# Kernel tuning notes

Measured on AMD Instinct MI355X. Metric: run time of the kernel, lower is better.

## Reference

```python
import jax, jax.numpy as jnp
import numpy as np

N = 50000    # nodes
R = 3        # relations
E = 600000   # edges per relation
IN, HID, OUT = 128, 64, 64


def setup_inputs() -> dict:
    key = jax.random.key(0)
    k = jax.random.split(key, 5)
    x = jax.random.normal(k[0], (N, IN), dtype=jnp.float32)
    src = jax.random.randint(k[1], (R, E), 0, N, dtype=jnp.int32)
    dst = jax.random.randint(k[2], (R, E), 0, N, dtype=jnp.int32)
    # glorot-ish init like dgl.nn.GraphConv weight; bias init zeros
    W1 = jax.random.normal(k[3], (R, IN, HID), dtype=jnp.float32) * (IN ** -0.5)
    b1 = jnp.zeros((R, HID), dtype=jnp.float32)
    W2 = jax.random.normal(k[4], (R, HID, OUT), dtype=jnp.float32) * (HID ** -0.5)
    b2 = jnp.zeros((R, OUT), dtype=jnp.float32)
    return {"x": x, "W1": W1, "b1": b1, "W2": W2, "b2": b2, "src": src, "dst": dst}


def _graph_conv(x, src, dst, W, b):
    """dgl.nn.GraphConv with norm='both', single relation.
    x: [N, Fin]; src/dst: [E] int; W: [Fin, Fout]; b: [Fout].
    """
    n = x.shape[0]
    ones = jnp.ones(src.shape[0], dtype=x.dtype)
    out_deg = jax.ops.segment_sum(ones, src, num_segments=n)
    h = x * (jnp.maximum(out_deg, 1.0) ** -0.5)[:, None]   # src-side norm
    if W.shape[0] > W.shape[1]:
        # mult W first, then aggregate (fewer flops per edge)
        h = h @ W
        agg = jax.ops.segment_sum(h[src], dst, num_segments=n)  # [N, Fout]
    else:
        agg = jax.ops.segment_sum(h[src], dst, num_segments=n) @ W
    in_deg = jax.ops.segment_sum(ones, dst, num_segments=n)
    return agg * (jnp.maximum(in_deg, 1.0) ** -0.5)[:, None] + b


def _hetero_conv(x, src, dst, W, b):
    # HeteroGraphConv(aggregate='sum'): run each relation's GraphConv, sum results.
    per_rel = jax.vmap(_graph_conv, in_axes=(None, 0, 0, 0, 0))(x, src, dst, W, b)
    return per_rel.sum(axis=0)  # [N, Fout]


def reference(x, W1, b1, W2, b2, src, dst):
    h = jax.nn.relu(_hetero_conv(x, src, dst, W1, b1))
    return _hetero_conv(h, src, dst, W2, b2)
```

## Files before the change

kernel.cpp:

```cpp
#include <hip/hip_runtime.h>

#define NODES 50000
#define RELS  3
#define NEDGE 600000
#define FIN   128
#define FHID  64
#define FOUT  64
#define SEGS  (RELS * NODES)

#define HC     96
#define HCHUNK (NEDGE / HC)
#define HBYTES NODES
#define HWORDS (HBYTES / 4)

#define BS     250
#define NBUK   200
#define NBUKT  (RELS * NBUK)
#define CAPLOG 12
#define CAP    (1 << CAPLOG)
#define BCH    192
#define BCHUNK (NEDGE / BCH)

typedef _Float16 half8 __attribute__((ext_vector_type(8)));
typedef float   floatx4 __attribute__((ext_vector_type(4)));

__global__ __launch_bounds__(1024) void hist_kernel(const int* __restrict__ src,
                                                    unsigned int* __restrict__ slab32,
                                                    int* __restrict__ bcur,
                                                    const float* __restrict__ W1,
                                                    const float* __restrict__ W2,
                                                    _Float16* __restrict__ W1t,
                                                    _Float16* __restrict__ W2t) {
    __shared__ unsigned int bins[HWORDS];
    int chunk = blockIdx.x, r = blockIdx.y;
    const int* arr = src + (size_t)r * NEDGE + (size_t)chunk * HCHUNK;
    for (int w = threadIdx.x; w < HWORDS; w += 1024) bins[w] = 0u;
    __syncthreads();
    for (int i = threadIdx.x; i < HCHUNK; i += 1024) {
        int v = arr[i];
        atomicAdd(&bins[v >> 2], 1u << ((v & 3) * 8));
    }
    __syncthreads();
    unsigned int* out = slab32 + ((size_t)(r * HC + chunk)) * HWORDS;
    for (int w = threadIdx.x; w < HWORDS; w += 1024) out[w] = bins[w];

    if (r == 0) {
        int gid = chunk * 1024 + threadIdx.x;
        if (gid < NBUKT) bcur[gid] = 0;
        int g2 = gid - 1024;
        if (g2 >= 0 && g2 < RELS * FIN * FHID) {
            int rr = g2 / (FIN * FHID);
            int rem = g2 - rr * FIN * FHID;
            int k = rem / FHID, j = rem - k * FHID;
            W1t[((size_t)rr * FHID + j) * FIN + k] = (_Float16)W1[g2];
            return;
        }
        int g3 = g2 - RELS * FIN * FHID;
        if (g3 >= 0 && g3 < RELS * FHID * FOUT) {
            int rr = g3 / (FHID * FOUT);
            int rem = g3 - rr * FHID * FOUT;
            int k = rem / FOUT, j = rem - k * FOUT;
            W2t[((size_t)rr * FOUT + j) * FHID + k] = (_Float16)W2[g3];
        }
    }
}

__global__ __launch_bounds__(512) void bucketize_kernel(const int* __restrict__ src,
                                                        const int* __restrict__ dst,
                                                        int* __restrict__ bcur,
                                                        unsigned int* __restrict__ rec) {
    __shared__ unsigned int stage[BCHUNK];
    __shared__ int bh[NBUK], bbase[NBUK], blc[NBUK];
    int chunk = blockIdx.x, r = blockIdx.y;
    for (int i = threadIdx.x; i < NBUK; i += 512) { bh[i] = 0; blc[i] = 0; }
    __syncthreads();
    size_t ebase = (size_t)r * NEDGE + (size_t)chunk * BCHUNK;
    for (int i = threadIdx.x; i < BCHUNK; i += 512) {
        int d = dst[ebase + i], s = src[ebase + i];
        int b = d / BS;
        int dl = d - b * BS;
        stage[i] = ((unsigned)s << 16) | ((unsigned)b << 8) | (unsigned)dl;
        atomicAdd(&bh[b], 1);
    }
    __syncthreads();
    for (int i = threadIdx.x; i < NBUK; i += 512)
        bbase[i] = atomicAdd(&bcur[r * NBUK + i], bh[i]);
    __syncthreads();
    for (int i = threadIdx.x; i < BCHUNK; i += 512) {
        unsigned u = stage[i];
        int b = (u >> 8) & 255;
        int slot = bbase[b] + atomicAdd(&blc[b], 1);
        rec[(((size_t)r * NBUK + b) << CAPLOG) + slot] = u;
    }
}

__global__ __launch_bounds__(512) void degfill_kernel(const unsigned int* __restrict__ rec,
                                                      const int* __restrict__ bcur,
                                                      const unsigned char* __restrict__ slab8,
                                                      int* __restrict__ idI,
                                                      float* __restrict__ innorm,
                                                      float* __restrict__ outnorm,
                                                      int* __restrict__ offs,
                                                      unsigned short* __restrict__ edge_src) {
    __shared__ int cnt[BS], lcur[BS], obase[BS];
    __shared__ int red[512];
    int tid = threadIdx.x;
    int b = blockIdx.x, r = blockIdx.y;
    int gbid = r * NBUK + b;
    for (int i = tid; i < BS; i += 512) { cnt[i] = 0; lcur[i] = 0; }
    __syncthreads();
    int n = bcur[gbid];
    const unsigned int* rb = rec + ((size_t)gbid << CAPLOG);
    for (int i = tid; i < n; i += 512) atomicAdd(&cnt[rb[i] & 255], 1);
    int p = 0;
    for (int i = tid; i < gbid; i += 512) p += bcur[i];
    red[tid] = p;
    __syncthreads();
    for (int off = 256; off > 0; off >>= 1) {
        if (tid < off) red[tid] += red[tid + off];
        __syncthreads();
    }
    int bpre = red[0];
    int v = (tid < BS) ? cnt[tid] : 0;
    __syncthreads();
    red[tid] = v;
    __syncthreads();
    for (int off = 1; off < 512; off <<= 1) {
        int add = (tid >= off) ? red[tid - off] : 0;
        __syncthreads();
        red[tid] += add;
        __syncthreads();
    }
    int segbase = r * NODES + b * BS;
    if (tid < BS) {
        int o = bpre + (red[tid] - v);
        obase[tid] = o;
        offs[segbase + tid] = o;
        idI[segbase + tid] = v;
        innorm[segbase + tid] = rsqrtf(fmaxf((float)v, 1.0f));
        int od = 0;
        const unsigned char* sl = slab8 + (size_t)r * HC * HBYTES + b * BS;
#pragma unroll 4
        for (int ch = 0; ch < HC; ++ch) od += sl[(size_t)ch * HBYTES + tid];
        outnorm[segbase + tid] = rsqrtf(fmaxf((float)od, 1.0f));
    }
    __syncthreads();
    for (int i = tid; i < n; i += 512) {
        unsigned u = rb[i];
        int dl = u & 255;
        int pos = obase[dl] + atomicAdd(&lcur[dl], 1);
        edge_src[pos] = (unsigned short)(u >> 16);
    }
}

__global__ __launch_bounds__(256, 4) void gemm1_kernel(const float* __restrict__ x,
                                                       const _Float16* __restrict__ W1t,
                                                       const float* __restrict__ outnorm,
                                                       _Float16* __restrict__ h) {
    int lane = threadIdx.x & 63;
    int wv   = threadIdx.x >> 6;
    int m = lane & 15, quad = lane >> 4;
    int n0 = (blockIdx.x * 4 + wv) * 16;
    if (n0 + 16 > NODES) n0 = NODES - 16;
    const float* xrow = x + (size_t)(n0 + m) * FIN + quad * 8;

    floatx4 acc[12];
#pragma unroll
    for (int t = 0; t < 12; ++t) acc[t] = (floatx4){0.f, 0.f, 0.f, 0.f};

#pragma unroll 1
    for (int ks = 0; ks < 4; ++ks) {
        float4 xa = *(const float4*)(xrow + ks * 32);
        float4 xb = *(const float4*)(xrow + ks * 32 + 4);
        half8 a;
        a[0] = (_Float16)xa.x; a[1] = (_Float16)xa.y;
        a[2] = (_Float16)xa.z; a[3] = (_Float16)xa.w;
        a[4] = (_Float16)xb.x; a[5] = (_Float16)xb.y;
        a[6] = (_Float16)xb.z; a[7] = (_Float16)xb.w;
#pragma unroll
        for (int jt = 0; jt < 12; ++jt) {
            const _Float16* bp = W1t + ((size_t)jt * 16 + m) * FIN + ks * 32 + quad * 8;
            half8 b = *(const half8*)bp;
            acc[jt] = __builtin_amdgcn_mfma_f32_16x16x32_f16(a, b, acc[jt], 0, 0, 0);
        }
    }

#pragma unroll
    for (int jt = 0; jt < 12; ++jt) {
        int r = jt >> 2;
        int j = (jt & 3) * 16 + m;
        _Float16* hb = h + (size_t)r * NODES * FHID;
        const float* on = outnorm + r * NODES;
#pragma unroll
        for (int reg = 0; reg < 4; ++reg) {
            int node = n0 + quad * 4 + reg;
            hb[(size_t)node * FHID + j] = (_Float16)(acc[jt][reg] * on[node]);
        }
    }
}

__device__ __forceinline__ void seg_sum8(const _Float16* __restrict__ hb,
                                         const unsigned short* __restrict__ es,
                                         int o, int c, int q, float* __restrict__ s) {
#pragma unroll
    for (int i = 0; i < 8; ++i) s[i] = 0.f;
    int t = 0;
    for (; t + 8 <= c; t += 8) {
        int ix[8];
        half8 v[8];
#pragma unroll
        for (int k = 0; k < 8; ++k) ix[k] = es[o + t + k];
#pragma unroll
        for (int k = 0; k < 8; ++k) v[k] = *(const half8*)(hb + (size_t)ix[k] * FHID + q * 8);
#pragma unroll
        for (int k = 0; k < 8; ++k)
#pragma unroll
            for (int i = 0; i < 8; ++i) s[i] += (float)v[k][i];
    }
    if (t + 4 <= c) {
        int ix[4];
        half8 v[4];
#pragma unroll
        for (int k = 0; k < 4; ++k) ix[k] = es[o + t + k];
#pragma unroll
        for (int k = 0; k < 4; ++k) v[k] = *(const half8*)(hb + (size_t)ix[k] * FHID + q * 8);
#pragma unroll
        for (int k = 0; k < 4; ++k)
#pragma unroll
            for (int i = 0; i < 8; ++i) s[i] += (float)v[k][i];
        t += 4;
    }
    if (t + 2 <= c) {
        int i0 = es[o + t], i1 = es[o + t + 1];
        half8 v0 = *(const half8*)(hb + (size_t)i0 * FHID + q * 8);
        half8 v1 = *(const half8*)(hb + (size_t)i1 * FHID + q * 8);
#pragma unroll
        for (int i = 0; i < 8; ++i) {
            s[i] += (float)v0[i];
            s[i] += (float)v1[i];
        }
        t += 2;
    }
    if (t < c) {
        int i0 = es[o + t];
        half8 v0 = *(const half8*)(hb + (size_t)i0 * FHID + q * 8);
#pragma unroll
        for (int i = 0; i < 8; ++i) s[i] += (float)v0[i];
    }
}

__global__ __launch_bounds__(256) void gather1_kernel(const _Float16* __restrict__ h,
                                                      const unsigned short* __restrict__ es,
                                                      const int* __restrict__ offs,
                                                      const int* __restrict__ cnt,
                                                      const float* __restrict__ innorm,
                                                      const float* __restrict__ b1,
                                                      _Float16* __restrict__ B) {
    int lane = threadIdx.x & 63;
    int wv   = threadIdx.x >> 6;
    int w    = blockIdx.x * 4 + wv;
    if (w * 8 >= NODES) return;
    int q    = lane & 7;
    int e8   = lane >> 3;
    int d    = w * 8 + e8;
    int c0 = cnt[d], c1 = cnt[NODES + d], c2 = cnt[2 * NODES + d];
    int o0 = offs[d], o1 = offs[NODES + d], o2 = offs[2 * NODES + d];
    float w0 = innorm[d], w1 = innorm[NODES + d], w2 = innorm[2 * NODES + d];

    float tot[8], s[8];
    seg_sum8(h, es, o0, c0, q, s);
#pragma unroll
    for (int i = 0; i < 8; ++i) tot[i] = w0 * s[i];
    seg_sum8(h + (size_t)NODES * FHID, es, o1, c1, q, s);
#pragma unroll
    for (int i = 0; i < 8; ++i) tot[i] = fmaf(w1, s[i], tot[i]);
    seg_sum8(h + 2 * (size_t)NODES * FHID, es, o2, c2, q, s);
#pragma unroll
    for (int i = 0; i < 8; ++i) tot[i] = fmaf(w2, s[i], tot[i]);

    half8 o8;
#pragma unroll
    for (int i = 0; i < 8; ++i) {
        int j = q * 8 + i;
        float bs = b1[j] + b1[FHID + j] + b1[2 * FHID + j];
        o8[i] = (_Float16)fmaxf(tot[i] + bs, 0.f);
    }
    *(half8*)(B + (size_t)d * FHID + q * 8) = o8;
}

__global__ __launch_bounds__(256) void gather2_kernel(const _Float16* __restrict__ h1,
                                                      const unsigned short* __restrict__ es,
                                                      const int* __restrict__ offs,
                                                      const int* __restrict__ cnt,
                                                      const float* __restrict__ outnorm,
                                                      const float* __restrict__ innorm,
                                                      _Float16* __restrict__ A2) {
    int lane = threadIdx.x & 63;
    int wv   = threadIdx.x >> 6;
    int w    = blockIdx.x * 4 + wv;
    int s0   = w * 8;
    if (s0 >= SEGS) return;
    int q    = lane & 7;
    int e8   = lane >> 3;
    int seg  = s0 + e8;
    int o = offs[seg], c = cnt[seg];
    const float* on = outnorm + (s0 / NODES) * NODES;

    float tot[8];
#pragma unroll
    for (int i = 0; i < 8; ++i) tot[i] = 0.f;
    int t = 0;
    for (; t + 8 <= c; t += 8) {
        int ix[8];
        float wk[8];
        half8 v[8];
#pragma unroll
        for (int k = 0; k < 8; ++k) ix[k] = es[o + t + k];
#pragma unroll
        for (int k = 0; k < 8; ++k) wk[k] = on[ix[k]];
#pragma unroll
        for (int k = 0; k < 8; ++k) v[k] = *(const half8*)(h1 + (size_t)ix[k] * FHID + q * 8);
#pragma unroll
        for (int k = 0; k < 8; ++k)
#pragma unroll
            for (int i = 0; i < 8; ++i) tot[i] = fmaf(wk[k], (float)v[k][i], tot[i]);
    }
    if (t + 4 <= c) {
        int ix[4];
        float wk[4];
        half8 v[4];
#pragma unroll
        for (int k = 0; k < 4; ++k) ix[k] = es[o + t + k];
#pragma unroll
        for (int k = 0; k < 4; ++k) wk[k] = on[ix[k]];
#pragma unroll
        for (int k = 0; k < 4; ++k) v[k] = *(const half8*)(h1 + (size_t)ix[k] * FHID + q * 8);
#pragma unroll
        for (int k = 0; k < 4; ++k)
#pragma unroll
            for (int i = 0; i < 8; ++i) tot[i] = fmaf(wk[k], (float)v[k][i], tot[i]);
        t += 4;
    }
    if (t + 2 <= c) {
        int i0 = es[o + t], i1 = es[o + t + 1];
        float w0 = on[i0], w1 = on[i1];
        half8 v0 = *(const half8*)(h1 + (size_t)i0 * FHID + q * 8);
        half8 v1 = *(const half8*)(h1 + (size_t)i1 * FHID + q * 8);
#pragma unroll
        for (int i = 0; i < 8; ++i) {
            tot[i] = fmaf(w0, (float)v0[i], tot[i]);
            tot[i] = fmaf(w1, (float)v1[i], tot[i]);
        }
        t += 2;
    }
    if (t < c) {
        int i0 = es[o + t];
        float w0 = on[i0];
        half8 v0 = *(const half8*)(h1 + (size_t)i0 * FHID + q * 8);
#pragma unroll
        for (int i = 0; i < 8; ++i) tot[i] = fmaf(w0, (float)v0[i], tot[i]);
    }

    float inr = innorm[seg];
    half8 o8;
#pragma unroll
    for (int i = 0; i < 8; ++i) o8[i] = (_Float16)(inr * tot[i]);
    *(half8*)(A2 + (size_t)seg * FHID + q * 8) = o8;
}

__global__ __launch_bounds__(256, 4) void out_kernel(const _Float16* __restrict__ A2,
                                                     const _Float16* __restrict__ W2t,
                                                     const float* __restrict__ b2,
                                                     float* __restrict__ out) {
    int lane = threadIdx.x & 63;
    int wv   = threadIdx.x >> 6;
    int m = lane & 15, quad = lane >> 4;
    int n0 = (blockIdx.x * 4 + wv) * 16;
    if (n0 + 16 > NODES) n0 = NODES - 16;

    floatx4 acc[4];
#pragma unroll
    for (int t = 0; t < 4; ++t) acc[t] = (floatx4){0.f, 0.f, 0.f, 0.f};

#pragma unroll 1
    for (int kk = 0; kk < 6; ++kk) {
        int r = kk >> 1, kb = (kk & 1) * 32;
        const _Float16* ap = A2 + ((size_t)r * NODES + n0 + m) * FHID + kb + quad * 8;
        half8 a = *(const half8*)ap;
#pragma unroll
        for (int jt = 0; jt < 4; ++jt) {
            const _Float16* bp = W2t + ((size_t)(r * FOUT + jt * 16 + m)) * FHID + kb + quad * 8;
            half8 b = *(const half8*)bp;
            acc[jt] = __builtin_amdgcn_mfma_f32_16x16x32_f16(a, b, acc[jt], 0, 0, 0);
        }
    }

#pragma unroll
    for (int jt = 0; jt < 4; ++jt) {
        int j = jt * 16 + m;
        float bs = b2[j] + b2[FOUT + j] + b2[2 * FOUT + j];
#pragma unroll
        for (int reg = 0; reg < 4; ++reg) {
            int node = n0 + quad * 4 + reg;
            out[(size_t)node * FOUT + j] = acc[jt][reg] + bs;
        }
    }
}

extern "C" void kernel_launch(void* const* d_in, const int* in_sizes, int n_in,
                              void* d_out, int out_size, void* d_ws, size_t ws_size,
                              hipStream_t stream) {
    const float* x   = (const float*)d_in[0];
    const float* W1  = (const float*)d_in[1];
    const float* b1  = (const float*)d_in[2];
    const float* W2  = (const float*)d_in[3];
    const float* b2  = (const float*)d_in[4];
    const int*   src = (const int*)d_in[5];
    const int*   dst = (const int*)d_in[6];
    float* out = (float*)d_out;

    int*   idI      = (int*)d_ws;
    int*   offs     = idI + SEGS;
    int*   bcur     = offs + SEGS;
    unsigned short* edge_src = (unsigned short*)(bcur + 1024);
    float* outnorm  = (float*)(edge_src + (size_t)RELS * NEDGE);
    float* innorm   = outnorm + SEGS;
    _Float16* W1t   = (_Float16*)(innorm + SEGS);
    _Float16* W2t   = W1t + (size_t)RELS * FHID * FIN;
    _Float16* h     = W2t + (size_t)RELS * FHID * FOUT;
    _Float16* B     = h + (size_t)SEGS * FHID;
    _Float16* A2    = B + (size_t)NODES * FHID;
    unsigned int*  rec    = (unsigned int*)h;
    unsigned int*  slab32 = rec + (size_t)NBUKT * CAP;
    unsigned char* slab8  = (unsigned char*)slab32;

    const int GW = ((NODES / 16) + 4) / 4;

    hist_kernel<<<dim3(HC, RELS), 1024, 0, stream>>>(src, slab32, bcur, W1, W2, W1t, W2t);
    bucketize_kernel<<<dim3(BCH, RELS), 512, 0, stream>>>(src, dst, bcur, rec);
    degfill_kernel<<<dim3(NBUK, RELS), 512, 0, stream>>>(rec, bcur, slab8, idI, innorm,
                                                         outnorm, offs, edge_src);

    gemm1_kernel<<<GW, 256, 0, stream>>>(x, W1t, outnorm, h);
    gather1_kernel<<<(NODES / 8 + 3) / 4, 256, 0, stream>>>(h, edge_src, offs, idI, innorm, b1, B);

    gather2_kernel<<<(SEGS / 8 + 3) / 4, 256, 0, stream>>>(B, edge_src, offs, idI, outnorm, innorm, A2);
    out_kernel<<<GW, 256, 0, stream>>>(A2, W2t, b2, out);
}
```

Baseline: 238.5 us.

## Fuse histogram and bucketize kernels; loop relations inside gather2

Merges the source-degree histogram and the destination bucketization into one front kernel that reads src/dst once per chunk, then re-reads them for the scatter pass instead of staging in LDS. The bucket counter reset moves to a hipMemsetAsync. gather2 now has each wave handle all three relations for its 8 nodes, so it launches a third as many blocks. This saves a launch and some edge traffic, but the front kernel re-reads edges and does more work per block, and gather2 exposes less parallelism.

```diff
diff --git a/kernel.cpp b/kernel.cpp
--- a/kernel.cpp
+++ b/kernel.cpp
@@ -18,35 +18,48 @@
 #define NBUKT  (RELS * NBUK)
 #define CAPLOG 12
 #define CAP    (1 << CAPLOG)
-#define BCH    192
-#define BCHUNK (NEDGE / BCH)
 
 typedef _Float16 half8 __attribute__((ext_vector_type(8)));
 typedef float   floatx4 __attribute__((ext_vector_type(4)));
 
-__global__ __launch_bounds__(1024) void hist_kernel(const int* __restrict__ src,
-                                                    unsigned int* __restrict__ slab32,
-                                                    int* __restrict__ bcur,
-                                                    const float* __restrict__ W1,
-                                                    const float* __restrict__ W2,
-                                                    _Float16* __restrict__ W1t,
-                                                    _Float16* __restrict__ W2t) {
+__global__ __launch_bounds__(1024) void front_kernel(const int* __restrict__ src,
+                                                     const int* __restrict__ dst,
+                                                     unsigned int* __restrict__ slab32,
+                                                     int* __restrict__ bcur,
+                                                     unsigned int* __restrict__ rec,
+                                                     const float* __restrict__ W1,
+                                                     const float* __restrict__ W2,
+                                                     _Float16* __restrict__ W1t,
+                                                     _Float16* __restrict__ W2t) {
     __shared__ unsigned int bins[HWORDS];
+    __shared__ int bh[NBUK], bbase[NBUK], blc[NBUK];
+    int tid = threadIdx.x;
     int chunk = blockIdx.x, r = blockIdx.y;
-    const int* arr = src + (size_t)r * NEDGE + (size_t)chunk * HCHUNK;
-    for (int w = threadIdx.x; w < HWORDS; w += 1024) bins[w] = 0u;
-    __syncthreads();
-    for (int i = threadIdx.x; i < HCHUNK; i += 1024) {
-        int v = arr[i];
-        atomicAdd(&bins[v >> 2], 1u << ((v & 3) * 8));
-    }
-    __syncthreads();
-    unsigned int* out = slab32 + ((size_t)(r * HC + chunk)) * HWORDS;
-    for (int w = threadIdx.x; w < HWORDS; w += 1024) out[w] = bins[w];
-
+    for (int i = tid; i < HWORDS; i += 1024) bins[i] = 0u;
+    for (int i = tid; i < NBUK; i += 1024) { bh[i] = 0; blc[i] = 0; }
+    __syncthreads();
+    size_t ebase = (size_t)r * NEDGE + (size_t)chunk * HCHUNK;
+    for (int i = tid; i < HCHUNK; i += 1024) {
+        int s = src[ebase + i], d = dst[ebase + i];
+        atomicAdd(&bins[s >> 2], 1u << ((s & 3) * 8));
+        atomicAdd(&bh[d / BS], 1);
+    }
+    __syncthreads();
+    unsigned int* outp = slab32 + ((size_t)(r * HC + chunk)) * HWORDS;
+    for (int i = tid; i < HWORDS; i += 1024) outp[i] = bins[i];
+    for (int i = tid; i < NBUK; i += 1024)
+        bbase[i] = atomicAdd(&bcur[r * NBUK + i], bh[i]);
+    __syncthreads();
+    for (int i = tid; i < HCHUNK; i += 1024) {
+        int s = src[ebase + i], d = dst[ebase + i];
+        int b = d / BS;
+        int dl = d - b * BS;
+        int slot = bbase[b] + atomicAdd(&blc[b], 1);
+        rec[(((size_t)r * NBUK + b) << CAPLOG) + slot] =
+            ((unsigned)s << 16) | ((unsigned)b << 8) | (unsigned)dl;
+    }
     if (r == 0) {
-        int gid = chunk * 1024 + threadIdx.x;
-        if (gid < NBUKT) bcur[gid] = 0;
+        int gid = chunk * 1024 + tid;
         int g2 = gid - 1024;
         if (g2 >= 0 && g2 < RELS * FIN * FHID) {
             int rr = g2 / (FIN * FHID);
@@ -62,35 +75,6 @@
             int k = rem / FOUT, j = rem - k * FOUT;
             W2t[((size_t)rr * FOUT + j) * FHID + k] = (_Float16)W2[g3];
         }
-    }
-}
-
-__global__ __launch_bounds__(512) void bucketize_kernel(const int* __restrict__ src,
-                                                        const int* __restrict__ dst,
-                                                        int* __restrict__ bcur,
-                                                        unsigned int* __restrict__ rec) {
-    __shared__ unsigned int stage[BCHUNK];
-    __shared__ int bh[NBUK], bbase[NBUK], blc[NBUK];
-    int chunk = blockIdx.x, r = blockIdx.y;
-    for (int i = threadIdx.x; i < NBUK; i += 512) { bh[i] = 0; blc[i] = 0; }
-    __syncthreads();
-    size_t ebase = (size_t)r * NEDGE + (size_t)chunk * BCHUNK;
-    for (int i = threadIdx.x; i < BCHUNK; i += 512) {
-        int d = dst[ebase + i], s = src[ebase + i];
-        int b = d / BS;
-        int dl = d - b * BS;
-        stage[i] = ((unsigned)s << 16) | ((unsigned)b << 8) | (unsigned)dl;
-        atomicAdd(&bh[b], 1);
-    }
-    __syncthreads();
-    for (int i = threadIdx.x; i < NBUK; i += 512)
-        bbase[i] = atomicAdd(&bcur[r * NBUK + i], bh[i]);
-    __syncthreads();
-    for (int i = threadIdx.x; i < BCHUNK; i += 512) {
-        unsigned u = stage[i];
-        int b = (u >> 8) & 255;
-        int slot = bbase[b] + atomicAdd(&blc[b], 1);
-        rec[(((size_t)r * NBUK + b) << CAPLOG) + slot] = u;
     }
 }
 
@@ -246,6 +230,65 @@
         half8 v0 = *(const half8*)(hb + (size_t)i0 * FHID + q * 8);
 #pragma unroll
         for (int i = 0; i < 8; ++i) s[i] += (float)v0[i];
+    }
+}
+
+__device__ __forceinline__ void wseg_sum8(const _Float16* __restrict__ hb,
+                                          const unsigned short* __restrict__ es,
+                                          const float* __restrict__ on,
+                                          int o, int c, int q, float* __restrict__ tot) {
+#pragma unroll
+    for (int i = 0; i < 8; ++i) tot[i] = 0.f;
+    int t = 0;
+    for (; t + 8 <= c; t += 8) {
+        int ix[8];
+        float wk[8];
+        half8 v[8];
+#pragma unroll
+        for (int k = 0; k < 8; ++k) ix[k] = es[o + t + k];
+#pragma unroll
+        for (int k = 0; k < 8; ++k) wk[k] = on[ix[k]];
+#pragma unroll
+        for (int k = 0; k < 8; ++k) v[k] = *(const half8*)(hb + (size_t)ix[k] * FHID + q * 8);
+#pragma unroll
+        for (int k = 0; k < 8; ++k)
+#pragma unroll
+            for (int i = 0; i < 8; ++i) tot[i] = fmaf(wk[k], (float)v[k][i], tot[i]);
+    }
+    if (t + 4 <= c) {
+        int ix[4];
+        float wk[4];
+        half8 v[4];
+#pragma unroll
+        for (int k = 0; k < 4; ++k) ix[k] = es[o + t + k];
+#pragma unroll
+        for (int k = 0; k < 4; ++k) wk[k] = on[ix[k]];
+#pragma unroll
+        for (int k = 0; k < 4; ++k) v[k] = *(const half8*)(hb + (size_t)ix[k] * FHID + q * 8);
+#pragma unroll
+        for (int k = 0; k < 4; ++k)
+#pragma unroll
+            for (int i = 0; i < 8; ++i) tot[i] = fmaf(wk[k], (float)v[k][i], tot[i]);
+        t += 4;
+    }
+    if (t + 2 <= c) {
+        int i0 = es[o + t], i1 = es[o + t + 1];
+        float w0 = on[i0], w1 = on[i1];
+        half8 v0 = *(const half8*)(hb + (size_t)i0 * FHID + q * 8);
+        half8 v1 = *(const half8*)(hb + (size_t)i1 * FHID + q * 8);
+#pragma unroll
+        for (int i = 0; i < 8; ++i) {
+            tot[i] = fmaf(w0, (float)v0[i], tot[i]);
+            tot[i] = fmaf(w1, (float)v1[i], tot[i]);
+        }
+        t += 2;
+    }
+    if (t < c) {
+        int i0 = es[o + t];
+        float w0 = on[i0];
+        half8 v0 = *(const half8*)(hb + (size_t)i0 * FHID + q * 8);
+#pragma unroll
+        for (int i = 0; i < 8; ++i) tot[i] = fmaf(w0, (float)v0[i], tot[i]);
     }
 }
 
@@ -298,74 +341,23 @@
     int lane = threadIdx.x & 63;
     int wv   = threadIdx.x >> 6;
     int w    = blockIdx.x * 4 + wv;
-    int s0   = w * 8;
-    if (s0 >= SEGS) return;
+    if (w * 8 >= NODES) return;
     int q    = lane & 7;
     int e8   = lane >> 3;
-    int seg  = s0 + e8;
-    int o = offs[seg], c = cnt[seg];
-    const float* on = outnorm + (s0 / NODES) * NODES;
+    int d    = w * 8 + e8;
 
     float tot[8];
-#pragma unroll
-    for (int i = 0; i < 8; ++i) tot[i] = 0.f;
-    int t = 0;
-    for (; t + 8 <= c; t += 8) {
-        int ix[8];
-        float wk[8];
-        half8 v[8];
-#pragma unroll
-        for (int k = 0; k < 8; ++k) ix[k] = es[o + t + k];
-#pragma unroll
-        for (int k = 0; k < 8; ++k) wk[k] = on[ix[k]];
-#pragma unroll
-        for (int k = 0; k < 8; ++k) v[k] = *(const half8*)(h1 + (size_t)ix[k] * FHID + q * 8);
-#pragma unroll
-        for (int k = 0; k < 8; ++k)
-#pragma unroll
-            for (int i = 0; i < 8; ++i) tot[i] = fmaf(wk[k], (float)v[k][i], tot[i]);
-    }
-    if (t + 4 <= c) {
-        int ix[4];
-        float wk[4];
-        half8 v[4];
-#pragma unroll
-        for (int k = 0; k < 4; ++k) ix[k] = es[o + t + k];
-#pragma unroll
-        for (int k = 0; k < 4; ++k) wk[k] = on[ix[k]];
-#pragma unroll
-        for (int k = 0; k < 4; ++k) v[k] = *(const half8*)(h1 + (size_t)ix[k] * FHID + q * 8);
-#pragma unroll
-        for (int k = 0; k < 4; ++k)
-#pragma unroll
-            for (int i = 0; i < 8; ++i) tot[i] = fmaf(wk[k], (float)v[k][i], tot[i]);
-        t += 4;
-    }
-    if (t + 2 <= c) {
-        int i0 = es[o + t], i1 = es[o + t + 1];
-        float w0 = on[i0], w1 = on[i1];
-        half8 v0 = *(const half8*)(h1 + (size_t)i0 * FHID + q * 8);
-        half8 v1 = *(const half8*)(h1 + (size_t)i1 * FHID + q * 8);
-#pragma unroll
-        for (int i = 0; i < 8; ++i) {
-            tot[i] = fmaf(w0, (float)v0[i], tot[i]);
-            tot[i] = fmaf(w1, (float)v1[i], tot[i]);
-        }
-        t += 2;
-    }
-    if (t < c) {
-        int i0 = es[o + t];
-        float w0 = on[i0];
-        half8 v0 = *(const half8*)(h1 + (size_t)i0 * FHID + q * 8);
-#pragma unroll
-        for (int i = 0; i < 8; ++i) tot[i] = fmaf(w0, (float)v0[i], tot[i]);
-    }
-
-    float inr = innorm[seg];
-    half8 o8;
-#pragma unroll
-    for (int i = 0; i < 8; ++i) o8[i] = (_Float16)(inr * tot[i]);
-    *(half8*)(A2 + (size_t)seg * FHID + q * 8) = o8;
+#pragma unroll 1
+    for (int r = 0; r < RELS; ++r) {
+        int seg = r * NODES + d;
+        int o = offs[seg], c = cnt[seg];
+        wseg_sum8(h1, es, outnorm + r * NODES, o, c, q, tot);
+        float inr = innorm[seg];
+        half8 o8;
+#pragma unroll
+        for (int i = 0; i < 8; ++i) o8[i] = (_Float16)(inr * tot[i]);
+        *(half8*)(A2 + (size_t)seg * FHID + q * 8) = o8;
+    }
 }
 
 __global__ __launch_bounds__(256, 4) void out_kernel(const _Float16* __restrict__ A2,
@@ -436,14 +428,15 @@
 
     const int GW = ((NODES / 16) + 4) / 4;
 
-    hist_kernel<<<dim3(HC, RELS), 1024, 0, stream>>>(src, slab32, bcur, W1, W2, W1t, W2t);
-    bucketize_kernel<<<dim3(BCH, RELS), 512, 0, stream>>>(src, dst, bcur, rec);
+    hipMemsetAsync(bcur, 0, 1024 * sizeof(int), stream);
+    front_kernel<<<dim3(HC, RELS), 1024, 0, stream>>>(src, dst, slab32, bcur, rec,
+                                                      W1, W2, W1t, W2t);
     degfill_kernel<<<dim3(NBUK, RELS), 512, 0, stream>>>(rec, bcur, slab8, idI, innorm,
                                                          outnorm, offs, edge_src);
 
     gemm1_kernel<<<GW, 256, 0, stream>>>(x, W1t, outnorm, h);
     gather1_kernel<<<(NODES / 8 + 3) / 4, 256, 0, stream>>>(h, edge_src, offs, idI, innorm, b1, B);
 
-    gather2_kernel<<<(SEGS / 8 + 3) / 4, 256, 0, stream>>>(B, edge_src, offs, idI, outnorm, innorm, A2);
+    gather2_kernel<<<(NODES / 8 + 3) / 4, 256, 0, stream>>>(B, edge_src, offs, idI, outnorm, innorm, A2);
     out_kernel<<<GW, 256, 0, stream>>>(A2, W2t, b2, out);
 }
```

Result: slower. 245.6 us (+3.0%).
